# Optimization experiments

Measured on AMD Instinct MI355X. Metric: run time of the kernel, lower is better.

Reference implementation:

```python
import jax, jax.numpy as jnp
import numpy as np

TOTAL = 67108864      # flat length of values
N_SEG = 1048576       # number of jagged segments


def setup_inputs() -> dict:
    key = jax.random.key(0)
    k1, k2 = jax.random.split(key)
    values = jax.random.normal(k1, (TOTAL,), dtype=jnp.float32)
    # cumulative end-offsets: sorted, strictly within (0, TOTAL], last pinned to TOTAL
    prefix_sum = jnp.sort(jax.random.randint(k2, (N_SEG,), 1, TOTAL, dtype=jnp.int64))
    prefix_sum = prefix_sum.at[-1].set(TOTAL)
    return {"values": values, "prefix_sum": prefix_sum}


def reference(values, prefix_sum):
    """Jagged per-segment argmax.

    values: [total] flat concatenation of segments.
    prefix_sum: [n_seg] cumulative end offsets (prefix_sum[-1] == total).
    Returns: [n_seg] int32 global flat index of the (first) max element in
    each segment. Empty segments (duplicate offsets) get sentinel `total`.
    """
    total = values.shape[0]
    n_seg = prefix_sum.shape[0]
    pos = jnp.arange(total, dtype=jnp.int32)
    # element i belongs to the first segment whose end offset exceeds i
    ids = jnp.searchsorted(prefix_sum, pos, side="right")  # [total]
    # per-segment max value
    maxv = jax.ops.segment_max(values, ids, num_segments=n_seg)  # [n_seg]
    # first global index attaining the segment max
    cand = jnp.where(values == maxv[ids], pos, total)
    idx = jax.ops.segment_min(cand, ids, num_segments=n_seg)  # [n_seg]
    return idx
```

## Files before the change

### kernel.cpp

```cpp
#include <hip/hip_runtime.h>
#include <cstdint>


#define IMAX      0x7FFFFFFF
#define C_CHUNK   8192
#define CAP       256
#define INIT_PACK 0x007FFFFF00000000ull
#define NEG_INF   __int_as_float(0xFF800000u)

__device__ __forceinline__ unsigned long long pack_vi(float v, int idx) {
    unsigned u = __float_as_uint(v);
    u = (u & 0x80000000u) ? ~u : (u | 0x80000000u);
    return ((unsigned long long)u << 32) |
           (unsigned long long)(0xFFFFFFFFu - (unsigned)idx);
}
__device__ __forceinline__ int decode_idx(unsigned long long p) {
    if (p == INIT_PACK) return IMAX;
    return (int)(0xFFFFFFFFu - (unsigned)(p & 0xFFFFFFFFull));
}

template<int CTRL>
__device__ __forceinline__ float dpp_fmax(float v) {
    int moved = __builtin_amdgcn_update_dpp((int)0xFF800000, __float_as_int(v),
                                            CTRL, 0xF, 0xF, false);
    return fmaxf(v, __int_as_float(moved));
}
template<int CTRL>
__device__ __forceinline__ int dpp_imin(int v) {
    int moved = __builtin_amdgcn_update_dpp(IMAX, v, CTRL, 0xF, 0xF, false);
    return min(v, moved);
}
__device__ __forceinline__ int wave_argmax64(float bv, int bi) {
    float m = bv;
    m = dpp_fmax<0xB1>(m); m = dpp_fmax<0x4E>(m);
    m = dpp_fmax<0x124>(m); m = dpp_fmax<0x128>(m);
    float r0 = __int_as_float(__builtin_amdgcn_readlane(__float_as_int(m), 0));
    float r1 = __int_as_float(__builtin_amdgcn_readlane(__float_as_int(m), 16));
    float r2 = __int_as_float(__builtin_amdgcn_readlane(__float_as_int(m), 32));
    float r3 = __int_as_float(__builtin_amdgcn_readlane(__float_as_int(m), 48));
    float maxv = fmaxf(fmaxf(r0, r1), fmaxf(r2, r3));
    int cand = (bv == maxv) ? bi : IMAX;
    cand = dpp_imin<0xB1>(cand); cand = dpp_imin<0x4E>(cand);
    cand = dpp_imin<0x124>(cand); cand = dpp_imin<0x128>(cand);
    int i0 = __builtin_amdgcn_readlane(cand, 0);
    int i1 = __builtin_amdgcn_readlane(cand, 16);
    int i2 = __builtin_amdgcn_readlane(cand, 32);
    int i3 = __builtin_amdgcn_readlane(cand, 48);
    return min(min(i0, i1), min(i2, i3));
}

__global__ void prep_kernel(const int* __restrict__ ps32, int n_seg,
                            int nchunks, int2* __restrict__ cs,
                            int* __restrict__ psc) {
    int s = blockIdx.x * blockDim.x + threadIdx.x;
    if (s >= n_seg) return;
    const bool is64 = (ps32[1] == 0);
    const int  psw  = is64 ? 2 : 1;
    int hi_b = ps32[s * psw];
    int lo_b = s ? ps32[(s - 1) * psw] : 0;
    psc[s] = hi_b;
    int c_first = (lo_b + C_CHUNK - 1) / C_CHUNK;
    int c_last  = (hi_b - 1) / C_CHUNK;
    if (c_last >= nchunks) c_last = nchunks - 1;
    for (int c = c_first; c <= c_last; ++c)
        cs[c] = make_int2(s, lo_b);
}

__global__ __launch_bounds__(256) void jagged_main_kernel(
    const float* __restrict__ values,
    const int*   __restrict__ psc,
    int n_seg,
    int* __restrict__ out,
    const int2* __restrict__ cs,
    int nchunks)
{
    __shared__ int lds_ps[CAP + 1];
    __shared__ unsigned long long lds_res[CAP];
    __shared__ int sh_span;

    const int tid = (int)threadIdx.x;
    const int bid = (int)blockIdx.x;
    const int chunk = (bid & 7) * (nchunks >> 3) + (bid >> 3);
    const int c0 = chunk * C_CHUNK;
    const int chunkEnd = c0 + C_CHUNK;
    const int w = tid >> 6, l = tid & 63;

    const int2 sw = cs[chunk];
    const int s0 = sw.x, start0 = sw.y;

    const int sA = s0 + tid;
    const int bA = (sA < n_seg) ? psc[sA] : IMAX;

    const int mybase = c0 + (tid << 5);
    const float4* vp = (const float4*)(values + mybase);
    float4 e0 = vp[0], e1 = vp[1], e2 = vp[2], e3 = vp[3],
           e4 = vp[4], e5 = vp[5], e6 = vp[6], e7 = vp[7];

    lds_ps[tid]  = bA;
    lds_res[tid] = INIT_PACK;
    if (tid == 0) { lds_ps[CAP] = IMAX; sh_span = -1; }
    __syncthreads();

    int blo = 0, bhi = CAP;
    while (blo < bhi) {
        int mid = (blo + bhi) >> 1;
        if (lds_ps[mid] > mybase) bhi = mid; else blo = mid + 1;
    }
    int j = blo;
    int bnd = lds_ps[j];
    float bv = NEG_INF;
    int   bi = IMAX;

#define PROC_ELEM(VV, OFF)                                              \
    {                                                                   \
        int idx = mybase + (OFF);                                       \
        float v = (VV);                                                 \
        while (idx >= bnd) {                                            \
            if (bi != IMAX)                                             \
                atomicMax(&lds_res[min(j, CAP - 1)], pack_vi(bv, bi));  \
            bv = NEG_INF; bi = IMAX;                                    \
            ++j; bnd = lds_ps[min(j, CAP)];                             \
        }                                                               \
        if (v > bv) { bv = v; bi = idx; }                               \
    }
#define PROC4(R, E)                                                     \
    PROC_ELEM((E).x, (R)*4 + 0) PROC_ELEM((E).y, (R)*4 + 1)             \
    PROC_ELEM((E).z, (R)*4 + 2) PROC_ELEM((E).w, (R)*4 + 3)
    PROC4(0, e0) PROC4(1, e1) PROC4(2, e2) PROC4(3, e3)
    PROC4(4, e4) PROC4(5, e5) PROC4(6, e6) PROC4(7, e7)
#undef PROC4
#undef PROC_ELEM
    if (bi != IMAX) atomicMax(&lds_res[min(j, CAP - 1)], pack_vi(bv, bi));
    __syncthreads();

    {
        int s = s0 + tid;
        if (s < n_seg) {
            int end_b   = lds_ps[tid];
            int start_b = tid ? lds_ps[tid - 1] : start0;
            if (start_b == end_b) {
                if (start_b > c0 && start_b <= chunkEnd) out[s] = IMAX;
            } else if (start_b >= c0 && start_b < chunkEnd) {
                if (end_b <= chunkEnd) out[s] = decode_idx(lds_res[tid]);
                else sh_span = tid;
            }
        }
    }
    __syncthreads();

    const int span = sh_span;
    if (span >= 0 && w == 0) {
        int end_b   = lds_ps[span];
        int start_b = span ? lds_ps[span - 1] : start0;
        float sv = NEG_INF; int si = IMAX;
        for (int i = start_b + l; i < end_b; i += 64) {
            float v = values[i];
            if (v > sv) { sv = v; si = i; }
        }
        int idx = wave_argmax64(sv, si);
        if (l == 0) out[s0 + span] = idx;
    }
}

__device__ __forceinline__ void upd_pair(const float* __restrict__ values,
                                         int i, int end, float& bv, int& bi) {
    float v0 = (i     < end) ? values[i]     : NEG_INF;
    float v1 = (i + 1 < end) ? values[i + 1] : NEG_INF;
    if (v0 > bv) { bv = v0; bi = i; }
    if (v1 > bv) { bv = v1; bi = i + 1; }
}
__global__ __launch_bounds__(256) void jagged_fallback_kernel(
    const float* __restrict__ values, const int* __restrict__ ps32,
    int n_seg, int* __restrict__ out)
{
    const int pair = blockIdx.x * (blockDim.x >> 6) + ((int)threadIdx.x >> 6);
    const int lane = (int)threadIdx.x & 63;
    const int seg0 = pair * 2;
    if (seg0 >= n_seg) return;
    const bool has1 = (seg0 + 1) < n_seg;
    const bool is64 = (ps32[1] == 0);
    const long long* ps64 = (const long long*)ps32;
    int s0, e0, e1;
    if (is64) { s0 = seg0 ? (int)ps64[seg0-1] : 0; e0 = (int)ps64[seg0];
                e1 = has1 ? (int)ps64[seg0+1] : e0; }
    else      { s0 = seg0 ? ps32[seg0-1] : 0; e0 = ps32[seg0];
                e1 = has1 ? ps32[seg0+1] : e0; }
    float bv0 = NEG_INF, bv1 = NEG_INF; int bi0 = IMAX, bi1 = IMAX;
    upd_pair(values, s0 + 2*lane, e0, bv0, bi0);
    upd_pair(values, e0 + 2*lane, e1, bv1, bi1);
    for (int i = s0 + 2*lane + 128; i < e0; i += 128) upd_pair(values, i, e0, bv0, bi0);
    for (int i = e0 + 2*lane + 128; i < e1; i += 128) upd_pair(values, i, e1, bv1, bi1);
    int idx0 = wave_argmax64(bv0, bi0);
    int idx1 = wave_argmax64(bv1, bi1);
    int myi = (lane == 0) ? idx0 : idx1;
    if (lane < (has1 ? 2 : 1)) out[seg0 + lane] = myi;
}

extern "C" void kernel_launch(void* const* d_in, const int* in_sizes, int n_in,
                              void* d_out, int out_size, void* d_ws, size_t ws_size,
                              hipStream_t stream) {
    const float* values = (const float*)d_in[0];
    const int*   ps32   = (const int*)d_in[1];
    const int n_seg = in_sizes[1];
    const int total = in_sizes[0];
    int* out = (int*)d_out;

    const int nchunks = total / C_CHUNK;
    const size_t need = (size_t)nchunks * sizeof(int2) + (size_t)n_seg * 4;
    if ((total % C_CHUNK) == 0 && (nchunks % 8) == 0 && n_seg >= 2 &&
        ws_size >= need) {
        int2* cs = (int2*)d_ws;
        int*  psc = (int*)((char*)d_ws + (size_t)nchunks * sizeof(int2));
        prep_kernel<<<(n_seg + 255) / 256, 256, 0, stream>>>(
            ps32, n_seg, nchunks, cs, psc);
        jagged_main_kernel<<<nchunks, 256, 0, stream>>>(
            values, psc, n_seg, out, cs, nchunks);
    } else {
        const int segs_per_block = 8;
        const int grid = (n_seg + segs_per_block - 1) / segs_per_block;
        jagged_fallback_kernel<<<grid, 256, 0, stream>>>(values, ps32, n_seg, out);
    }
}
```

Before: 54.54 us.

## Drop prep kernel; locate chunk start segment via in-kernel wave-parallel search

Result: slower. 56.56 us (+3.7%).

```diff
diff --git a/kernel.cpp b/kernel.cpp
--- a/kernel.cpp
+++ b/kernel.cpp
@@ -5,6 +5,7 @@
 #define IMAX      0x7FFFFFFF
 #define C_CHUNK   8192
 #define CAP       256
+#define BRK       2048
 #define INIT_PACK 0x007FFFFF00000000ull
 #define NEG_INF   __int_as_float(0xFF800000u)
 
@@ -49,29 +50,12 @@
     return min(min(i0, i1), min(i2, i3));
 }
 
-__global__ void prep_kernel(const int* __restrict__ ps32, int n_seg,
-                            int nchunks, int2* __restrict__ cs,
-                            int* __restrict__ psc) {
-    int s = blockIdx.x * blockDim.x + threadIdx.x;
-    if (s >= n_seg) return;
-    const bool is64 = (ps32[1] == 0);
-    const int  psw  = is64 ? 2 : 1;
-    int hi_b = ps32[s * psw];
-    int lo_b = s ? ps32[(s - 1) * psw] : 0;
-    psc[s] = hi_b;
-    int c_first = (lo_b + C_CHUNK - 1) / C_CHUNK;
-    int c_last  = (hi_b - 1) / C_CHUNK;
-    if (c_last >= nchunks) c_last = nchunks - 1;
-    for (int c = c_first; c <= c_last; ++c)
-        cs[c] = make_int2(s, lo_b);
-}
-
 __global__ __launch_bounds__(256) void jagged_main_kernel(
     const float* __restrict__ values,
-    const int*   __restrict__ psc,
+    const int*   __restrict__ ps32,
     int n_seg,
+    int total,
     int* __restrict__ out,
-    const int2* __restrict__ cs,
     int nchunks)
 {
     __shared__ int lds_ps[CAP + 1];
@@ -85,11 +69,35 @@
     const int chunkEnd = c0 + C_CHUNK;
     const int w = tid >> 6, l = tid & 63;
 
-    const int2 sw = cs[chunk];
-    const int s0 = sw.x, start0 = sw.y;
+    const bool is64 = (ps32[1] == 0);
+    const int  psw  = is64 ? 2 : 1;
+
+    int m = (int)((long long)c0 * (long long)n_seg / (long long)total);
+    int blo = max(0, m - BRK);
+    int bhi = min(n_seg - 1, m + BRK);
+    while (blo > 0 && ps32[(blo - 1) * psw] > c0) {
+        bhi = blo - 1;
+        blo = max(0, blo - 4 * BRK);
+    }
+    while (ps32[bhi * psw] <= c0) {
+        blo = bhi + 1;
+        bhi = min(n_seg - 1, bhi + 4 * BRK);
+    }
+    while (bhi > blo) {
+        int step = (bhi - blo + 63) >> 6;
+        int pos  = min(blo + l * step, bhi);
+        bool cond = ps32[pos * psw] > c0;
+        unsigned long long msk = __ballot(cond);
+        int f = (int)__builtin_ctzll(msk);
+        int nbhi = min(blo + f * step, bhi);
+        int nblo = (f == 0) ? blo : min(blo + (f - 1) * step, bhi) + 1;
+        bhi = nbhi; blo = nblo;
+    }
+    const int s0 = blo;
+    const int start0 = s0 ? ps32[(s0 - 1) * psw] : 0;
 
     const int sA = s0 + tid;
-    const int bA = (sA < n_seg) ? psc[sA] : IMAX;
+    const int bA = (sA < n_seg) ? ps32[sA * psw] : IMAX;
 
     const int mybase = c0 + (tid << 5);
     const float4* vp = (const float4*)(values + mybase);
@@ -101,12 +109,12 @@
     if (tid == 0) { lds_ps[CAP] = IMAX; sh_span = -1; }
     __syncthreads();
 
-    int blo = 0, bhi = CAP;
-    while (blo < bhi) {
-        int mid = (blo + bhi) >> 1;
-        if (lds_ps[mid] > mybase) bhi = mid; else blo = mid + 1;
-    }
-    int j = blo;
+    int qlo = 0, qhi = CAP;
+    while (qlo < qhi) {
+        int mid = (qlo + qhi) >> 1;
+        if (lds_ps[mid] > mybase) qhi = mid; else qlo = mid + 1;
+    }
+    int j = qlo;
     int bnd = lds_ps[j];
     float bv = NEG_INF;
     int   bi = IMAX;
@@ -206,15 +214,9 @@
     int* out = (int*)d_out;
 
     const int nchunks = total / C_CHUNK;
-    const size_t need = (size_t)nchunks * sizeof(int2) + (size_t)n_seg * 4;
-    if ((total % C_CHUNK) == 0 && (nchunks % 8) == 0 && n_seg >= 2 &&
-        ws_size >= need) {
-        int2* cs = (int2*)d_ws;
-        int*  psc = (int*)((char*)d_ws + (size_t)nchunks * sizeof(int2));
-        prep_kernel<<<(n_seg + 255) / 256, 256, 0, stream>>>(
-            ps32, n_seg, nchunks, cs, psc);
+    if ((total % C_CHUNK) == 0 && (nchunks % 8) == 0 && n_seg >= 2) {
         jagged_main_kernel<<<nchunks, 256, 0, stream>>>(
-            values, psc, n_seg, out, cs, nchunks);
+            values, ps32, n_seg, total, out, nchunks);
     } else {
         const int segs_per_block = 8;
         const int grid = (n_seg + segs_per_block - 1) / segs_per_block;
```
